# Kernel optimization log

Hardware: AMD Instinct MI355X
Metric: run time of the kernel (lower is better)

Reference implementation:

```python
import jax, jax.numpy as jnp
import numpy as np

BLOCK_LEN = 64

def _segsum(x):
    # x: (..., T) -> (..., T, T) with entry [t, s] = sum_{u=s+1..t} x[u], -inf above diagonal
    T = x.shape[-1]
    cs = jnp.cumsum(x, axis=-1)
    ss = cs[..., :, None] - cs[..., None, :]
    mask = jnp.tril(jnp.ones((T, T), dtype=bool))
    return jnp.where(mask, ss, -jnp.inf)

def setup_inputs() -> dict:
    key = jax.random.key(0)
    kx, ka, kb, kc = jax.random.split(key, 4)
    b, L, h, p, n = 4, 4096, 32, 64, 16
    X = jax.random.normal(kx, (b, L, h, p), dtype=jnp.float32)
    # negative, small-magnitude A so exp(cumsum(A)) stays finite (decaying SSM),
    # matching the math of the module while keeping the baseline numerically sane
    A = -0.1 * jnp.abs(jax.random.normal(ka, (b, L, h), dtype=jnp.float32))
    B = jax.random.normal(kb, (b, L, h, n), dtype=jnp.float32)
    C = jax.random.normal(kc, (b, L, h, n), dtype=jnp.float32)
    return {"X": X, "A": A, "B": B, "C": C}

def reference(X, A, B, C):
    b, L, h, p = X.shape
    n = B.shape[-1]
    l = BLOCK_LEN
    c = L // l
    # chunk into blocks
    Xb = X.reshape(b, c, l, h, p)                       # b c l h p
    Ab = A.reshape(b, c, l, h).transpose(0, 3, 1, 2)    # b h c l
    Bb = B.reshape(b, c, l, h, n)                       # b c l h n
    Cb = C.reshape(b, c, l, h, n)                       # b c l h n
    A_cumsum = jnp.cumsum(Ab, axis=-1)                  # b h c l
    # intra-chunk (diagonal) term; equals the fused per-timestep scan
    # h_t = exp(A_t)*h_{t-1} + B_t*x_t ; y_t = C_t . h_t
    Lmat = jnp.exp(_segsum(Ab))                         # b h c l l (lower-tri)
    Y_diag = jnp.einsum('bclhn,bcshn,bhcls,bcshp->bclhp', Cb, Bb, Lmat, Xb)
    # per-chunk end states
    decay_states = jnp.exp(A_cumsum[..., -1:] - A_cumsum)  # b h c l
    states = jnp.einsum('bclhn,bhcl,bclhp->bchpn', Bb, decay_states, Xb)
    states = jnp.concatenate([jnp.zeros_like(states[:, :1]), states], axis=1)  # b (c+1) h p n
    # inter-chunk recurrence via segment-sum of chunk totals
    decay_chunk = jnp.exp(_segsum(jnp.pad(A_cumsum[..., -1], ((0, 0), (0, 0), (1, 0)))))  # b h (c+1) (c+1)
    new_states = jnp.einsum('bhzc,bchpn->bzhpn', decay_chunk, states)
    states = new_states[:, :-1]                          # b c h p n
    # state -> output contribution
    state_decay_out = jnp.exp(A_cumsum)                  # b h c l
    Y_off = jnp.einsum('bclhn,bchpn,bhcl->bclhp', Cb, states, state_decay_out)
    return (Y_diag + Y_off).reshape(b, L, h, p)
```

## Files before the change

kernel.cpp:

```cpp
#include <hip/hip_runtime.h>

#define BATCH   4
#define SEQLEN  4096
#define NHEADS  32
#define PDIM    64
#define NDIM    16
#define CHUNK   64
#define NCHUNK  64
#define PHALF   32

typedef short v8s __attribute__((ext_vector_type(8)));
typedef float v4f __attribute__((ext_vector_type(4)));

union V8U { v8s s; unsigned u[4]; };

__device__ __forceinline__ short f2bf(float f) {
    union { float f; unsigned u; } x; x.f = f;
    unsigned r = (x.u + 0x7FFFu + ((x.u >> 16) & 1u)) >> 16;
    return (short)r;
}
__device__ __forceinline__ float bf2f(short s) {
    union { unsigned u; float f; } x; x.u = ((unsigned)(unsigned short)s) << 16;
    return x.f;
}
__device__ __forceinline__ unsigned cvt_pk_bf16(float lo, float hi) {
    unsigned r;
    asm("v_cvt_pk_bf16_f32 %0, %1, %2" : "=v"(r) : "v"(lo), "v"(hi));
    return r;
}

__device__ __forceinline__ float wave_iscan(float v, int lane) {
#pragma unroll
    for (int d = 1; d < 64; d <<= 1) {
        float o = __shfl_up(v, (unsigned)d, 64);
        if (lane >= d) v += o;
    }
    return v;
}

__global__ __launch_bounds__(512) void k_fused(
    const float* __restrict__ X, const float* __restrict__ A,
    const float* __restrict__ Bm, const float* __restrict__ Cm,
    float* __restrict__ Y)
{
    const int ph = blockIdx.x, hh = blockIdx.y, bb = blockIdx.z;
    const int tid = threadIdx.x;
    const int lane = tid & 63;
    const int wv = tid >> 6;
    const int W = wv & 3;
    const int qq = lane >> 4, nn = lane & 15;

    __shared__ __align__(16) short xF [2][4][64][8];
    __shared__ __align__(16) short xSF[2][4][64][8];
    __shared__ __align__(16) short cFq[2][2048];
    __shared__ __align__(16) short bFq[2][2048];
    __shared__ __align__(16) short bFs[2][1024];
    __shared__ __align__(16) short sF [2][1024];
    __shared__ __align__(16) float gRaw[CHUNK][68];
    __shared__ float sCum[2][CHUNK];

    {
        const v8s z8 = {0,0,0,0,0,0,0,0};
        ((v8s*)cFq)[tid] = z8;
        ((v8s*)bFq)[tid] = z8;
        if (tid < 256) ((v8s*)sF)[tid] = z8;
    }

    auto stage = [&](int c, int buf) {
        const int t0c = bb * SEQLEN + c * CHUNK;
        const float af = A[(size_t)(t0c + lane) * NHEADS + hh];
        float cum = wave_iscan(af, lane);
        const float tot = __shfl(cum, 63, 64);
        if (wv == 4) sCum[buf][lane] = cum;
        const float dec_own = __expf(tot - cum);
        const int ti = wv - 4;
        const int kk = ti >> 1, nt = ti & 1;
        const int p = ph * PHALF + nt * 16 + nn;
        const float* xb = X + ((size_t)(t0c + kk * 32 + qq * 8) * NHEADS + hh) * PDIM + p;
        float xv[8];
#pragma unroll
        for (int j = 0; j < 8; ++j) xv[j] = xb[(size_t)j * NHEADS * PDIM];
        float dv[8];
#pragma unroll
        for (int j = 0; j < 8; ++j) dv[j] = __shfl(dec_own, kk * 32 + qq * 8 + j, 64);
        V8U xf, xs;
#pragma unroll
        for (int j2 = 0; j2 < 4; ++j2) {
            xf.u[j2] = cvt_pk_bf16(xv[2*j2], xv[2*j2+1]);
            xs.u[j2] = cvt_pk_bf16(xv[2*j2] * dv[2*j2], xv[2*j2+1] * dv[2*j2+1]);
        }
        *(v8s*)&xF [buf][kk*2+nt][lane][0] = xf.s;
        *(v8s*)&xSF[buf][kk*2+nt][lane][0] = xs.s;
        const int ptid = tid & 255;
        const int r = ptid >> 2, n0 = (ptid & 3) * 4;
        const float4 bv = *(const float4*)&Bm[((size_t)(t0c + r) * NHEADS + hh) * NDIM + n0];
        const int offq = ((r >> 4) * 64 + (n0 >> 3) * 16 + (r & 15)) * 8 + (n0 & 7);
        bFq[buf][offq + 0] = f2bf(bv.x); bFq[buf][offq + 1] = f2bf(bv.y);
        bFq[buf][offq + 2] = f2bf(bv.z); bFq[buf][offq + 3] = f2bf(bv.w);
        const int kb = r >> 5, qb = (r >> 3) & 3, jj = r & 7;
        const int bs = (kb * 64 + qb * 16) * 8 + jj;
        bFs[buf][bs + (n0 + 0) * 8] = f2bf(bv.x);
        bFs[buf][bs + (n0 + 1) * 8] = f2bf(bv.y);
        bFs[buf][bs + (n0 + 2) * 8] = f2bf(bv.z);
        bFs[buf][bs + (n0 + 3) * 8] = f2bf(bv.w);
        const float4 cv = *(const float4*)&Cm[((size_t)(t0c + r) * NHEADS + hh) * NDIM + n0];
        cFq[buf][offq + 0] = f2bf(cv.x); cFq[buf][offq + 1] = f2bf(cv.y);
        cFq[buf][offq + 2] = f2bf(cv.z); cFq[buf][offq + 3] = f2bf(cv.w);
    };

    __syncthreads();
    if (wv >= 4) stage(0, 0);
    __syncthreads();

    v4f S = {0.f, 0.f, 0.f, 0.f};
    const v4f zero = {0.f, 0.f, 0.f, 0.f};

#pragma unroll 1
    for (int k = 0; k < NCHUNK; ++k) {
        const int cur = k & 1;
        if (wv >= 4) {
            if (k + 1 < NCHUNK) stage(k + 1, cur ^ 1);
        } else {
            const int t0c = bb * SEQLEN + k * CHUNK;
            const float* scm = &sCum[cur][0];
            float tcum[4];
#pragma unroll
            for (int r = 0; r < 4; ++r) tcum[r] = scm[W * 16 + qq * 4 + r];
            const v8s cfrag = *(const v8s*)&cFq[cur][(W * 64 + lane) * 8];

#pragma unroll
            for (int st = 0; st < 4; ++st) {
                if (st <= W) {
                    const v8s bfrag = *(const v8s*)&bFq[cur][(st * 64 + lane) * 8];
                    v4f acc = __builtin_amdgcn_mfma_f32_16x16x32_bf16(cfrag, bfrag, zero, 0, 0, 0);
                    const float cums = scm[st * 16 + nn];
#pragma unroll
                    for (int r = 0; r < 4; ++r) {
                        const int t = W * 16 + qq * 4 + r;
                        const int s = st * 16 + nn;
                        gRaw[t][s] = (t >= s) ? acc[r] * __expf(tcum[r] - cums) : 0.f;
                    }
                }
            }
            if (W == 0) {
#pragma unroll
                for (int r = 0; r < 4; ++r) gRaw[qq * 4 + r][16 + nn] = 0.f;
            } else if (W == 2) {
#pragma unroll
                for (int r = 0; r < 4; ++r) gRaw[32 + qq * 4 + r][48 + nn] = 0.f;
            }

            const float et = __expf(scm[W * 16 + nn]);
            V8U cef;
#pragma unroll
            for (int j2 = 0; j2 < 4; ++j2)
                cef.u[j2] = cvt_pk_bf16(bf2f(cfrag[2*j2]) * et, bf2f(cfrag[2*j2+1]) * et);

            V8U ga0u, ga1u;
            {
                const float* gr = &gRaw[W * 16 + nn][qq * 8];
#pragma unroll
                for (int j2 = 0; j2 < 4; ++j2) ga0u.u[j2] = cvt_pk_bf16(gr[2*j2], gr[2*j2+1]);
            }
            const bool usekk1 = (W >= 2);
            if (usekk1) {
                const float* gr = &gRaw[W * 16 + nn][32 + qq * 8];
#pragma unroll
                for (int j2 = 0; j2 < 4; ++j2) ga1u.u[j2] = cvt_pk_bf16(gr[2*j2], gr[2*j2+1]);
            }

            v4f ya[2];
#pragma unroll
            for (int nt2 = 0; nt2 < 2; ++nt2) {
                const v8s sfrag = *(const v8s*)&sF[cur][(nt2 * 64 + lane) * 8];
                v4f a = __builtin_amdgcn_mfma_f32_16x16x32_bf16(cef.s, sfrag, zero, 0, 0, 0);
                const v8s x0 = *(const v8s*)&xF[cur][0 + nt2][lane][0];
                a = __builtin_amdgcn_mfma_f32_16x16x32_bf16(ga0u.s, x0, a, 0, 0, 0);
                if (usekk1) {
                    const v8s x1 = *(const v8s*)&xF[cur][2 + nt2][lane][0];
                    a = __builtin_amdgcn_mfma_f32_16x16x32_bf16(ga1u.s, x1, a, 0, 0, 0);
                }
                ya[nt2] = a;
            }
#pragma unroll
            for (int r = 0; r < 4; ++r) {
                const int t = W * 16 + qq * 4 + r;
                float* yp = Y + ((size_t)(t0c + t) * NHEADS + hh) * PDIM + ph * PHALF + nn;
                yp[0]  = ya[0][r];
                yp[16] = ya[1][r];
            }

            if (W < 2) {
                const v8s a0 = *(const v8s*)&xSF[cur][0 + W][lane][0];
                const v8s a1 = *(const v8s*)&xSF[cur][2 + W][lane][0];
                const v8s b0 = *(const v8s*)&bFs[cur][(0 * 64 + lane) * 8];
                const v8s b1 = *(const v8s*)&bFs[cur][(1 * 64 + lane) * 8];
                v4f sa = __builtin_amdgcn_mfma_f32_16x16x32_bf16(a0, b0, zero, 0, 0, 0);
                sa = __builtin_amdgcn_mfma_f32_16x16x32_bf16(a1, b1, sa, 0, 0, 0);
                const float Et = __expf(scm[63]);
#pragma unroll
                for (int r = 0; r < 4; ++r) S[r] = Et * S[r] + sa[r];
                short* d = &sF[cur ^ 1][0];
#pragma unroll
                for (int r = 0; r < 4; ++r)
                    d[(W * 64 + (nn >> 3) * 16 + qq * 4 + r) * 8 + (nn & 7)] = f2bf(S[r]);
            }
        }
        __syncthreads();
    }
}

extern "C" void kernel_launch(void* const* d_in, const int* in_sizes, int n_in,
                              void* d_out, int out_size, void* d_ws, size_t ws_size,
                              hipStream_t stream) {
    const float* X  = (const float*)d_in[0];
    const float* A  = (const float*)d_in[1];
    const float* Bm = (const float*)d_in[2];
    const float* Cm = (const float*)d_in[3];
    float* Y = (float*)d_out;
    (void)d_ws; (void)ws_size;

    dim3 grid(2, NHEADS, BATCH);
    k_fused<<<grid, 512, 0, stream>>>(X, A, Bm, Cm, Y);
}
```

Baseline: 336.1 us.

## Split P into quarters, precompute full A cumsum, specialize staging waves

Doubles the grid by splitting the P dimension into four 16-wide slices, so each block handles a quarter of the head dimension and the workgroup count rises from 256 to 512. The cumulative sum of A over the whole sequence is computed once per block into shared memory, replacing the per-chunk wave scans, and chunk decays are formed relative to the previous chunk's cumsum. The staging waves are reassigned: two load X, one loads B and one loads C using contiguous float4 loads. In exchange, the per-chunk B·C gram MFMA work and the B/C loads are duplicated across twice as many blocks, and a global cumsum may lose float precision over long sequences.

```diff
diff --git a/kernel.cpp b/kernel.cpp
--- a/kernel.cpp
+++ b/kernel.cpp
@@ -7,7 +7,7 @@
 #define NDIM    16
 #define CHUNK   64
 #define NCHUNK  64
-#define PHALF   32
+#define PQ      16
 
 typedef short v8s __attribute__((ext_vector_type(8)));
 typedef float v4f __attribute__((ext_vector_type(4)));
@@ -50,65 +50,102 @@
     const int W = wv & 3;
     const int qq = lane >> 4, nn = lane & 15;
 
-    __shared__ __align__(16) short xF [2][4][64][8];
-    __shared__ __align__(16) short xSF[2][4][64][8];
+    __shared__ __align__(16) float sCumAll[SEQLEN];
+    __shared__ __align__(16) short xF [2][2][64][8];
+    __shared__ __align__(16) short xSF[2][2][64][8];
     __shared__ __align__(16) short cFq[2][2048];
     __shared__ __align__(16) short bFq[2][2048];
     __shared__ __align__(16) short bFs[2][1024];
-    __shared__ __align__(16) short sF [2][1024];
+    __shared__ __align__(16) short sF [2][512];
     __shared__ __align__(16) float gRaw[CHUNK][68];
-    __shared__ float sCum[2][CHUNK];
+    __shared__ float wtot[8];
 
     {
         const v8s z8 = {0,0,0,0,0,0,0,0};
         ((v8s*)cFq)[tid] = z8;
         ((v8s*)bFq)[tid] = z8;
-        if (tid < 256) ((v8s*)sF)[tid] = z8;
+        if (tid < 128) ((v8s*)sF)[tid] = z8;
+    }
+
+    {
+        const float* Ab = A + (size_t)bb * SEQLEN * NHEADS + hh;
+        const int tb = wv * 512 + lane * 8;
+        float av[8];
+#pragma unroll
+        for (int j = 0; j < 8; ++j) av[j] = Ab[(size_t)(tb + j) * NHEADS];
+        float s8 = 0.f;
+#pragma unroll
+        for (int j = 0; j < 8; ++j) s8 += av[j];
+        const float pre = wave_iscan(s8, lane);
+        if (lane == 63) wtot[wv] = pre;
+        __syncthreads();
+        float base = 0.f;
+#pragma unroll
+        for (int w = 0; w < 7; ++w) if (w < wv) base += wtot[w];
+        float c = base + pre - s8;
+#pragma unroll
+        for (int j = 0; j < 8; ++j) { c += av[j]; sCumAll[tb + j] = c; }
+        __syncthreads();
     }
 
     auto stage = [&](int c, int buf) {
         const int t0c = bb * SEQLEN + c * CHUNK;
-        const float af = A[(size_t)(t0c + lane) * NHEADS + hh];
-        float cum = wave_iscan(af, lane);
-        const float tot = __shfl(cum, 63, 64);
-        if (wv == 4) sCum[buf][lane] = cum;
-        const float dec_own = __expf(tot - cum);
-        const int ti = wv - 4;
-        const int kk = ti >> 1, nt = ti & 1;
-        const int p = ph * PHALF + nt * 16 + nn;
-        const float* xb = X + ((size_t)(t0c + kk * 32 + qq * 8) * NHEADS + hh) * PDIM + p;
-        float xv[8];
-#pragma unroll
-        for (int j = 0; j < 8; ++j) xv[j] = xb[(size_t)j * NHEADS * PDIM];
-        float dv[8];
-#pragma unroll
-        for (int j = 0; j < 8; ++j) dv[j] = __shfl(dec_own, kk * 32 + qq * 8 + j, 64);
-        V8U xf, xs;
-#pragma unroll
-        for (int j2 = 0; j2 < 4; ++j2) {
-            xf.u[j2] = cvt_pk_bf16(xv[2*j2], xv[2*j2+1]);
-            xs.u[j2] = cvt_pk_bf16(xv[2*j2] * dv[2*j2], xv[2*j2+1] * dv[2*j2+1]);
+        const float* gcc = &sCumAll[c * CHUNK];
+        if (wv <= 5) {
+            const int kk = wv - 4;
+            const int trow = kk * 32 + qq * 8;
+            const float* xb = X + ((size_t)(t0c + trow) * NHEADS + hh) * PDIM + ph * PQ + nn;
+            float xv[8];
+#pragma unroll
+            for (int j = 0; j < 8; ++j) xv[j] = xb[(size_t)j * (NHEADS * PDIM)];
+            const float gtot = gcc[63];
+            float ex[8];
+#pragma unroll
+            for (int j = 0; j < 8; ++j) ex[j] = __expf(gtot - gcc[trow + j]);
+            V8U xf, xs;
+#pragma unroll
+            for (int j2 = 0; j2 < 4; ++j2) {
+                xf.u[j2] = cvt_pk_bf16(xv[2*j2], xv[2*j2+1]);
+                xs.u[j2] = cvt_pk_bf16(xv[2*j2] * ex[2*j2], xv[2*j2+1] * ex[2*j2+1]);
+            }
+            *(v8s*)&xF [buf][kk][lane][0] = xf.s;
+            *(v8s*)&xSF[buf][kk][lane][0] = xs.s;
+        } else if (wv == 6) {
+            const float* bp = &Bm[((size_t)(t0c + lane) * NHEADS + hh) * NDIM];
+            const float4 v0 = *(const float4*)(bp);
+            const float4 v1 = *(const float4*)(bp + 4);
+            const float4 v2 = *(const float4*)(bp + 8);
+            const float4 v3 = *(const float4*)(bp + 12);
+            V8U lo, hi;
+            lo.u[0] = cvt_pk_bf16(v0.x, v0.y); lo.u[1] = cvt_pk_bf16(v0.z, v0.w);
+            lo.u[2] = cvt_pk_bf16(v1.x, v1.y); lo.u[3] = cvt_pk_bf16(v1.z, v1.w);
+            hi.u[0] = cvt_pk_bf16(v2.x, v2.y); hi.u[1] = cvt_pk_bf16(v2.z, v2.w);
+            hi.u[2] = cvt_pk_bf16(v3.x, v3.y); hi.u[3] = cvt_pk_bf16(v3.z, v3.w);
+            const int off0 = ((lane >> 4) * 64 + (lane & 15)) * 8;
+            *(v8s*)&bFq[buf][off0]       = lo.s;
+            *(v8s*)&bFq[buf][off0 + 128] = hi.s;
+            const int bs = ((lane >> 5) * 64 + ((lane >> 3) & 3) * 16) * 8 + (lane & 7);
+#pragma unroll
+            for (int n = 0; n < 8; ++n) bFs[buf][bs + n * 8]       = lo.s[n];
+#pragma unroll
+            for (int n = 0; n < 8; ++n) bFs[buf][bs + (n + 8) * 8] = hi.s[n];
+        } else {
+            const float* cp = &Cm[((size_t)(t0c + lane) * NHEADS + hh) * NDIM];
+            const float4 v0 = *(const float4*)(cp);
+            const float4 v1 = *(const float4*)(cp + 4);
+            const float4 v2 = *(const float4*)(cp + 8);
+            const float4 v3 = *(const float4*)(cp + 12);
+            V8U lo, hi;
+            lo.u[0] = cvt_pk_bf16(v0.x, v0.y); lo.u[1] = cvt_pk_bf16(v0.z, v0.w);
+            lo.u[2] = cvt_pk_bf16(v1.x, v1.y); lo.u[3] = cvt_pk_bf16(v1.z, v1.w);
+            hi.u[0] = cvt_pk_bf16(v2.x, v2.y); hi.u[1] = cvt_pk_bf16(v2.z, v2.w);
+            hi.u[2] = cvt_pk_bf16(v3.x, v3.y); hi.u[3] = cvt_pk_bf16(v3.z, v3.w);
+            const int off0 = ((lane >> 4) * 64 + (lane & 15)) * 8;
+            *(v8s*)&cFq[buf][off0]       = lo.s;
+            *(v8s*)&cFq[buf][off0 + 128] = hi.s;
         }
-        *(v8s*)&xF [buf][kk*2+nt][lane][0] = xf.s;
-        *(v8s*)&xSF[buf][kk*2+nt][lane][0] = xs.s;
-        const int ptid = tid & 255;
-        const int r = ptid >> 2, n0 = (ptid & 3) * 4;
-        const float4 bv = *(const float4*)&Bm[((size_t)(t0c + r) * NHEADS + hh) * NDIM + n0];
-        const int offq = ((r >> 4) * 64 + (n0 >> 3) * 16 + (r & 15)) * 8 + (n0 & 7);
-        bFq[buf][offq + 0] = f2bf(bv.x); bFq[buf][offq + 1] = f2bf(bv.y);
-        bFq[buf][offq + 2] = f2bf(bv.z); bFq[buf][offq + 3] = f2bf(bv.w);
-        const int kb = r >> 5, qb = (r >> 3) & 3, jj = r & 7;
-        const int bs = (kb * 64 + qb * 16) * 8 + jj;
-        bFs[buf][bs + (n0 + 0) * 8] = f2bf(bv.x);
-        bFs[buf][bs + (n0 + 1) * 8] = f2bf(bv.y);
-        bFs[buf][bs + (n0 + 2) * 8] = f2bf(bv.z);
-        bFs[buf][bs + (n0 + 3) * 8] = f2bf(bv.w);
-        const float4 cv = *(const float4*)&Cm[((size_t)(t0c + r) * NHEADS + hh) * NDIM + n0];
-        cFq[buf][offq + 0] = f2bf(cv.x); cFq[buf][offq + 1] = f2bf(cv.y);
-        cFq[buf][offq + 2] = f2bf(cv.z); cFq[buf][offq + 3] = f2bf(cv.w);
     };
 
-    __syncthreads();
     if (wv >= 4) stage(0, 0);
     __syncthreads();
 
@@ -122,10 +159,11 @@
             if (k + 1 < NCHUNK) stage(k + 1, cur ^ 1);
         } else {
             const int t0c = bb * SEQLEN + k * CHUNK;
-            const float* scm = &sCum[cur][0];
+            const float* gc = &sCumAll[k * CHUNK];
+            const float gbase = (k == 0) ? 0.f : gc[-1];
             float tcum[4];
 #pragma unroll
-            for (int r = 0; r < 4; ++r) tcum[r] = scm[W * 16 + qq * 4 + r];
+            for (int r = 0; r < 4; ++r) tcum[r] = gc[W * 16 + qq * 4 + r];
             const v8s cfrag = *(const v8s*)&cFq[cur][(W * 64 + lane) * 8];
 
 #pragma unroll
@@ -133,7 +171,7 @@
                 if (st <= W) {
                     const v8s bfrag = *(const v8s*)&bFq[cur][(st * 64 + lane) * 8];
                     v4f acc = __builtin_amdgcn_mfma_f32_16x16x32_bf16(cfrag, bfrag, zero, 0, 0, 0);
-                    const float cums = scm[st * 16 + nn];
+                    const float cums = gc[st * 16 + nn];
 #pragma unroll
                     for (int r = 0; r < 4; ++r) {
                         const int t = W * 16 + qq * 4 + r;
@@ -150,7 +188,7 @@
                 for (int r = 0; r < 4; ++r) gRaw[32 + qq * 4 + r][48 + nn] = 0.f;
             }
 
-            const float et = __expf(scm[W * 16 + nn]);
+            const float et = __expf(gc[W * 16 + nn] - gbase);
             V8U cef;
 #pragma unroll
             for (int j2 = 0; j2 < 4; ++j2)
@@ -169,41 +207,34 @@
                 for (int j2 = 0; j2 < 4; ++j2) ga1u.u[j2] = cvt_pk_bf16(gr[2*j2], gr[2*j2+1]);
             }
 
-            v4f ya[2];
-#pragma unroll
-            for (int nt2 = 0; nt2 < 2; ++nt2) {
-                const v8s sfrag = *(const v8s*)&sF[cur][(nt2 * 64 + lane) * 8];
-                v4f a = __builtin_amdgcn_mfma_f32_16x16x32_bf16(cef.s, sfrag, zero, 0, 0, 0);
-                const v8s x0 = *(const v8s*)&xF[cur][0 + nt2][lane][0];
-                a = __builtin_amdgcn_mfma_f32_16x16x32_bf16(ga0u.s, x0, a, 0, 0, 0);
-                if (usekk1) {
-                    const v8s x1 = *(const v8s*)&xF[cur][2 + nt2][lane][0];
-                    a = __builtin_amdgcn_mfma_f32_16x16x32_bf16(ga1u.s, x1, a, 0, 0, 0);
-                }
-                ya[nt2] = a;
+            const v8s sfrag = *(const v8s*)&sF[cur][lane * 8];
+            v4f a = __builtin_amdgcn_mfma_f32_16x16x32_bf16(cef.s, sfrag, zero, 0, 0, 0);
+            const v8s x0 = *(const v8s*)&xF[cur][0][lane][0];
+            a = __builtin_amdgcn_mfma_f32_16x16x32_bf16(ga0u.s, x0, a, 0, 0, 0);
+            if (usekk1) {
+                const v8s x1 = *(const v8s*)&xF[cur][1][lane][0];
+                a = __builtin_amdgcn_mfma_f32_16x16x32_bf16(ga1u.s, x1, a, 0, 0, 0);
             }
 #pragma unroll
             for (int r = 0; r < 4; ++r) {
                 const int t = W * 16 + qq * 4 + r;
-                float* yp = Y + ((size_t)(t0c + t) * NHEADS + hh) * PDIM + ph * PHALF + nn;
-                yp[0]  = ya[0][r];
-                yp[16] = ya[1][r];
-            }
-
-            if (W < 2) {
-                const v8s a0 = *(const v8s*)&xSF[cur][0 + W][lane][0];
-                const v8s a1 = *(const v8s*)&xSF[cur][2 + W][lane][0];
+                Y[((size_t)(t0c + t) * NHEADS + hh) * PDIM + ph * PQ + nn] = a[r];
+            }
+
+            if (W == 0) {
+                const v8s a0 = *(const v8s*)&xSF[cur][0][lane][0];
+                const v8s a1 = *(const v8s*)&xSF[cur][1][lane][0];
                 const v8s b0 = *(const v8s*)&bFs[cur][(0 * 64 + lane) * 8];
                 const v8s b1 = *(const v8s*)&bFs[cur][(1 * 64 + lane) * 8];
                 v4f sa = __builtin_amdgcn_mfma_f32_16x16x32_bf16(a0, b0, zero, 0, 0, 0);
                 sa = __builtin_amdgcn_mfma_f32_16x16x32_bf16(a1, b1, sa, 0, 0, 0);
-                const float Et = __expf(scm[63]);
+                const float Et = __expf(gc[63] - gbase);
 #pragma unroll
                 for (int r = 0; r < 4; ++r) S[r] = Et * S[r] + sa[r];
                 short* d = &sF[cur ^ 1][0];
 #pragma unroll
                 for (int r = 0; r < 4; ++r)
-                    d[(W * 64 + (nn >> 3) * 16 + qq * 4 + r) * 8 + (nn & 7)] = f2bf(S[r]);
+                    d[((nn >> 3) * 16 + qq * 4 + r) * 8 + (nn & 7)] = f2bf(S[r]);
             }
         }
         __syncthreads();
@@ -220,6 +251,6 @@
     float* Y = (float*)d_out;
     (void)d_ws; (void)ws_size;
 
-    dim3 grid(2, NHEADS, BATCH);
+    dim3 grid(4, NHEADS, BATCH);
     k_fused<<<grid, 512, 0, stream>>>(X, A, Bm, Cm, Y);
 }
```

Measured after the change: 367.4 us. 1.09x slower.

## Precompute global A cumsum, process chunk pairs with balanced triangular work and 4-deep buffers

Applied to the files above, without the earlier changes.

Computes the cumulative sum of A for the whole sequence once into shared memory, replacing the per-chunk wave scans in staging. The compute waves now handle two chunks per iteration: each wave builds the triangular G block for chunk A at row W and for chunk B at row 3-W, which balances the triangular MFMA work across waves. The state recurrence for both chunks runs before chunk B's output. Buffers go from double to quadruple, staging runs two chunks ahead, and s_setprio raises compute wave priority. Exponents now use differences from a global cumsum, so precision depends on that running sum, and shared memory use grows substantially.

```diff
diff --git a/kernel.cpp b/kernel.cpp
--- a/kernel.cpp
+++ b/kernel.cpp
@@ -50,44 +50,64 @@
     const int W = wv & 3;
     const int qq = lane >> 4, nn = lane & 15;
 
-    __shared__ __align__(16) short xF [2][4][64][8];
-    __shared__ __align__(16) short xSF[2][4][64][8];
-    __shared__ __align__(16) short cFq[2][2048];
-    __shared__ __align__(16) short bFq[2][2048];
-    __shared__ __align__(16) short bFs[2][1024];
-    __shared__ __align__(16) short sF [2][1024];
-    __shared__ __align__(16) float gRaw[CHUNK][68];
-    __shared__ float sCum[2][CHUNK];
+    __shared__ __align__(16) float sCumAll[SEQLEN];
+    __shared__ __align__(16) short xF [4][4][64][8];
+    __shared__ __align__(16) short xSF[4][4][64][8];
+    __shared__ __align__(16) short cFq[4][2048];
+    __shared__ __align__(16) short bFq[4][2048];
+    __shared__ __align__(16) short bFs[4][1024];
+    __shared__ __align__(16) short sF [4][1024];
+    __shared__ __align__(16) float gRawA[CHUNK][68];
+    __shared__ __align__(16) float gRawB[CHUNK][68];
+    __shared__ float wtot[8];
 
     {
         const v8s z8 = {0,0,0,0,0,0,0,0};
-        ((v8s*)cFq)[tid] = z8;
-        ((v8s*)bFq)[tid] = z8;
-        if (tid < 256) ((v8s*)sF)[tid] = z8;
+        ((v8s*)cFq)[tid] = z8; ((v8s*)cFq)[tid + 512] = z8;
+        ((v8s*)bFq)[tid] = z8; ((v8s*)bFq)[tid + 512] = z8;
+        if (tid < 128) ((v8s*)sF)[tid] = z8;
+    }
+
+    {
+        const float* Ab = A + (size_t)bb * SEQLEN * NHEADS + hh;
+        const int tb = wv * 512 + lane * 8;
+        float av[8];
+#pragma unroll
+        for (int j = 0; j < 8; ++j) av[j] = Ab[(size_t)(tb + j) * NHEADS];
+        float s8 = 0.f;
+#pragma unroll
+        for (int j = 0; j < 8; ++j) s8 += av[j];
+        const float pre = wave_iscan(s8, lane);
+        if (lane == 63) wtot[wv] = pre;
+        __syncthreads();
+        float base = 0.f;
+#pragma unroll
+        for (int w = 0; w < 7; ++w) if (w < wv) base += wtot[w];
+        float c = base + pre - s8;
+#pragma unroll
+        for (int j = 0; j < 8; ++j) { c += av[j]; sCumAll[tb + j] = c; }
+        __syncthreads();
     }
 
     auto stage = [&](int c, int buf) {
         const int t0c = bb * SEQLEN + c * CHUNK;
-        const float af = A[(size_t)(t0c + lane) * NHEADS + hh];
-        float cum = wave_iscan(af, lane);
-        const float tot = __shfl(cum, 63, 64);
-        if (wv == 4) sCum[buf][lane] = cum;
-        const float dec_own = __expf(tot - cum);
-        const int ti = wv - 4;
-        const int kk = ti >> 1, nt = ti & 1;
-        const int p = ph * PHALF + nt * 16 + nn;
-        const float* xb = X + ((size_t)(t0c + kk * 32 + qq * 8) * NHEADS + hh) * PDIM + p;
+        const float* gcc = &sCumAll[c * CHUNK];
+        const int ti = wv - 4, kk = ti >> 1, nt = ti & 1;
+        const int trow = kk * 32 + qq * 8;
+        const float* xb = X + ((size_t)(t0c + trow) * NHEADS + hh) * PDIM
+                            + ph * PHALF + nt * 16 + nn;
         float xv[8];
 #pragma unroll
-        for (int j = 0; j < 8; ++j) xv[j] = xb[(size_t)j * NHEADS * PDIM];
-        float dv[8];
-#pragma unroll
-        for (int j = 0; j < 8; ++j) dv[j] = __shfl(dec_own, kk * 32 + qq * 8 + j, 64);
+        for (int j = 0; j < 8; ++j) xv[j] = xb[(size_t)j * (NHEADS * PDIM)];
+        const float gtot = gcc[63];
+        float ex[8];
+#pragma unroll
+        for (int j = 0; j < 8; ++j) ex[j] = __expf(gtot - gcc[trow + j]);
         V8U xf, xs;
 #pragma unroll
         for (int j2 = 0; j2 < 4; ++j2) {
             xf.u[j2] = cvt_pk_bf16(xv[2*j2], xv[2*j2+1]);
-            xs.u[j2] = cvt_pk_bf16(xv[2*j2] * dv[2*j2], xv[2*j2+1] * dv[2*j2+1]);
+            xs.u[j2] = cvt_pk_bf16(xv[2*j2] * ex[2*j2], xv[2*j2+1] * ex[2*j2+1]);
         }
         *(v8s*)&xF [buf][kk*2+nt][lane][0] = xf.s;
         *(v8s*)&xSF[buf][kk*2+nt][lane][0] = xs.s;
@@ -108,103 +128,130 @@
         cFq[buf][offq + 2] = f2bf(cv.z); cFq[buf][offq + 3] = f2bf(cv.w);
     };
 
-    __syncthreads();
-    if (wv >= 4) stage(0, 0);
-    __syncthreads();
-
-    v4f S = {0.f, 0.f, 0.f, 0.f};
     const v4f zero = {0.f, 0.f, 0.f, 0.f};
 
-#pragma unroll 1
-    for (int k = 0; k < NCHUNK; ++k) {
-        const int cur = k & 1;
-        if (wv >= 4) {
-            if (k + 1 < NCHUNK) stage(k + 1, cur ^ 1);
-        } else {
-            const int t0c = bb * SEQLEN + k * CHUNK;
-            const float* scm = &sCum[cur][0];
-            float tcum[4];
-#pragma unroll
-            for (int r = 0; r < 4; ++r) tcum[r] = scm[W * 16 + qq * 4 + r];
-            const v8s cfrag = *(const v8s*)&cFq[cur][(W * 64 + lane) * 8];
-
-#pragma unroll
-            for (int st = 0; st < 4; ++st) {
-                if (st <= W) {
-                    const v8s bfrag = *(const v8s*)&bFq[cur][(st * 64 + lane) * 8];
-                    v4f acc = __builtin_amdgcn_mfma_f32_16x16x32_bf16(cfrag, bfrag, zero, 0, 0, 0);
-                    const float cums = scm[st * 16 + nn];
-#pragma unroll
-                    for (int r = 0; r < 4; ++r) {
-                        const int t = W * 16 + qq * 4 + r;
-                        const int s = st * 16 + nn;
-                        gRaw[t][s] = (t >= s) ? acc[r] * __expf(tcum[r] - cums) : 0.f;
-                    }
+    auto qk_g = [&](float (*gR)[68], const float* gc, int buf, int tau) -> v8s {
+        const v8s cfrag = *(const v8s*)&cFq[buf][(tau * 64 + lane) * 8];
+        float tc[4];
+#pragma unroll
+        for (int r = 0; r < 4; ++r) tc[r] = gc[tau * 16 + qq * 4 + r];
+#pragma unroll
+        for (int st = 0; st < 4; ++st) {
+            if (st <= tau) {
+                const v8s bfrag = *(const v8s*)&bFq[buf][(st * 64 + lane) * 8];
+                v4f acc = __builtin_amdgcn_mfma_f32_16x16x32_bf16(cfrag, bfrag, zero, 0, 0, 0);
+                const float cums = gc[st * 16 + nn];
+#pragma unroll
+                for (int r = 0; r < 4; ++r) {
+                    const int t = tau * 16 + qq * 4 + r;
+                    const int s = st * 16 + nn;
+                    gR[t][s] = (t >= s) ? acc[r] * __expf(tc[r] - cums) : 0.f;
                 }
             }
-            if (W == 0) {
-#pragma unroll
-                for (int r = 0; r < 4; ++r) gRaw[qq * 4 + r][16 + nn] = 0.f;
-            } else if (W == 2) {
-#pragma unroll
-                for (int r = 0; r < 4; ++r) gRaw[32 + qq * 4 + r][48 + nn] = 0.f;
+        }
+        if (tau == 0) {
+#pragma unroll
+            for (int r = 0; r < 4; ++r) gR[qq * 4 + r][16 + nn] = 0.f;
+        } else if (tau == 2) {
+#pragma unroll
+            for (int r = 0; r < 4; ++r) gR[32 + qq * 4 + r][48 + nn] = 0.f;
+        }
+        return cfrag;
+    };
+
+    auto do_y = [&](float (*gR)[68], const float* gc, float gbase, int buf,
+                    int t0c, v8s cfrag) {
+        const float et = __expf(gc[W * 16 + nn] - gbase);
+        V8U cef;
+#pragma unroll
+        for (int j2 = 0; j2 < 4; ++j2)
+            cef.u[j2] = cvt_pk_bf16(bf2f(cfrag[2*j2]) * et, bf2f(cfrag[2*j2+1]) * et);
+        V8U ga0u, ga1u;
+        {
+            const float* gr = &gR[W * 16 + nn][qq * 8];
+#pragma unroll
+            for (int j2 = 0; j2 < 4; ++j2) ga0u.u[j2] = cvt_pk_bf16(gr[2*j2], gr[2*j2+1]);
+        }
+        const bool usekk1 = (W >= 2);
+        if (usekk1) {
+            const float* gr = &gR[W * 16 + nn][32 + qq * 8];
+#pragma unroll
+            for (int j2 = 0; j2 < 4; ++j2) ga1u.u[j2] = cvt_pk_bf16(gr[2*j2], gr[2*j2+1]);
+        }
+        v4f ya[2];
+#pragma unroll
+        for (int nt2 = 0; nt2 < 2; ++nt2) {
+            const v8s sfrag = *(const v8s*)&sF[buf][(nt2 * 64 + lane) * 8];
+            v4f a = __builtin_amdgcn_mfma_f32_16x16x32_bf16(cef.s, sfrag, zero, 0, 0, 0);
+            const v8s x0 = *(const v8s*)&xF[buf][0 + nt2][lane][0];
+            a = __builtin_amdgcn_mfma_f32_16x16x32_bf16(ga0u.s, x0, a, 0, 0, 0);
+            if (usekk1) {
+                const v8s x1 = *(const v8s*)&xF[buf][2 + nt2][lane][0];
+                a = __builtin_amdgcn_mfma_f32_16x16x32_bf16(ga1u.s, x1, a, 0, 0, 0);
             }
-
-            const float et = __expf(scm[W * 16 + nn]);
-            V8U cef;
-#pragma unroll
-            for (int j2 = 0; j2 < 4; ++j2)
-                cef.u[j2] = cvt_pk_bf16(bf2f(cfrag[2*j2]) * et, bf2f(cfrag[2*j2+1]) * et);
-
-            V8U ga0u, ga1u;
-            {
-                const float* gr = &gRaw[W * 16 + nn][qq * 8];
-#pragma unroll
-                for (int j2 = 0; j2 < 4; ++j2) ga0u.u[j2] = cvt_pk_bf16(gr[2*j2], gr[2*j2+1]);
+            ya[nt2] = a;
+        }
+#pragma unroll
+        for (int r = 0; r < 4; ++r) {
+            const int t = W * 16 + qq * 4 + r;
+            float* yp = Y + ((size_t)(t0c + t) * NHEADS + hh) * PDIM + ph * PHALF + nn;
+            yp[0]  = ya[0][r];
+            yp[16] = ya[1][r];
+        }
+    };
+
+    auto do_state = [&](int buf, float Et, int pub, v4f& S) {
+        const v8s a0 = *(const v8s*)&xSF[buf][0 + W][lane][0];
+        const v8s a1 = *(const v8s*)&xSF[buf][2 + W][lane][0];
+        const v8s b0 = *(const v8s*)&bFs[buf][(0 * 64 + lane) * 8];
+        const v8s b1 = *(const v8s*)&bFs[buf][(1 * 64 + lane) * 8];
+        v4f sa = __builtin_amdgcn_mfma_f32_16x16x32_bf16(a0, b0, zero, 0, 0, 0);
+        sa = __builtin_amdgcn_mfma_f32_16x16x32_bf16(a1, b1, sa, 0, 0, 0);
+#pragma unroll
+        for (int r = 0; r < 4; ++r) S[r] = Et * S[r] + sa[r];
+        short* d = &sF[pub][0];
+#pragma unroll
+        for (int r = 0; r < 4; ++r)
+            d[(W * 64 + (nn >> 3) * 16 + qq * 4 + r) * 8 + (nn & 7)] = f2bf(S[r]);
+    };
+
+    if (wv >= 4) { stage(0, 0); stage(1, 1); }
+    __syncthreads();
+
+    v4f S = {0.f, 0.f, 0.f, 0.f};
+    v8s cfragB = {0,0,0,0,0,0,0,0};
+
+#pragma unroll 1
+    for (int k = 0; k < NCHUNK; k += 2) {
+        const int bufA = k & 3, bufB = (k + 1) & 3;
+        const float* gcA = &sCumAll[k * CHUNK];
+        const float* gcB = gcA + CHUNK;
+
+        if (wv >= 4) {
+            if (k + 2 < NCHUNK) stage(k + 2, (k + 2) & 3);
+        } else {
+            __builtin_amdgcn_s_setprio(1);
+            const float gbaseA = (k == 0) ? 0.f : gcA[-1];
+            const int t0cA = bb * SEQLEN + k * CHUNK;
+            const v8s cfragA = qk_g(gRawA, gcA, bufA, W);
+            qk_g(gRawB, gcB, bufB, 3 - W);
+            do_y(gRawA, gcA, gbaseA, bufA, t0cA, cfragA);
+            if (W < 2) {
+                do_state(bufA, __expf(gcA[63] - gbaseA), bufB, S);
+                do_state(bufB, __expf(gcB[63] - gcA[63]), (k + 2) & 3, S);
             }
-            const bool usekk1 = (W >= 2);
-            if (usekk1) {
-                const float* gr = &gRaw[W * 16 + nn][32 + qq * 8];
-#pragma unroll
-                for (int j2 = 0; j2 < 4; ++j2) ga1u.u[j2] = cvt_pk_bf16(gr[2*j2], gr[2*j2+1]);
-            }
-
-            v4f ya[2];
-#pragma unroll
-            for (int nt2 = 0; nt2 < 2; ++nt2) {
-                const v8s sfrag = *(const v8s*)&sF[cur][(nt2 * 64 + lane) * 8];
-                v4f a = __builtin_amdgcn_mfma_f32_16x16x32_bf16(cef.s, sfrag, zero, 0, 0, 0);
-                const v8s x0 = *(const v8s*)&xF[cur][0 + nt2][lane][0];
-                a = __builtin_amdgcn_mfma_f32_16x16x32_bf16(ga0u.s, x0, a, 0, 0, 0);
-                if (usekk1) {
-                    const v8s x1 = *(const v8s*)&xF[cur][2 + nt2][lane][0];
-                    a = __builtin_amdgcn_mfma_f32_16x16x32_bf16(ga1u.s, x1, a, 0, 0, 0);
-                }
-                ya[nt2] = a;
-            }
-#pragma unroll
-            for (int r = 0; r < 4; ++r) {
-                const int t = W * 16 + qq * 4 + r;
-                float* yp = Y + ((size_t)(t0c + t) * NHEADS + hh) * PDIM + ph * PHALF + nn;
-                yp[0]  = ya[0][r];
-                yp[16] = ya[1][r];
-            }
-
-            if (W < 2) {
-                const v8s a0 = *(const v8s*)&xSF[cur][0 + W][lane][0];
-                const v8s a1 = *(const v8s*)&xSF[cur][2 + W][lane][0];
-                const v8s b0 = *(const v8s*)&bFs[cur][(0 * 64 + lane) * 8];
-                const v8s b1 = *(const v8s*)&bFs[cur][(1 * 64 + lane) * 8];
-                v4f sa = __builtin_amdgcn_mfma_f32_16x16x32_bf16(a0, b0, zero, 0, 0, 0);
-                sa = __builtin_amdgcn_mfma_f32_16x16x32_bf16(a1, b1, sa, 0, 0, 0);
-                const float Et = __expf(scm[63]);
-#pragma unroll
-                for (int r = 0; r < 4; ++r) S[r] = Et * S[r] + sa[r];
-                short* d = &sF[cur ^ 1][0];
-#pragma unroll
-                for (int r = 0; r < 4; ++r)
-                    d[(W * 64 + (nn >> 3) * 16 + qq * 4 + r) * 8 + (nn & 7)] = f2bf(S[r]);
-            }
+            __builtin_amdgcn_s_setprio(0);
+        }
+        __syncthreads();
+
+        if (wv >= 4) {
+            if (k + 3 < NCHUNK) stage(k + 3, (k + 3) & 3);
+        } else {
+            __builtin_amdgcn_s_setprio(1);
+            const int t0cB = bb * SEQLEN + (k + 1) * CHUNK;
+            cfragB = *(const v8s*)&cFq[bufB][(W * 64 + lane) * 8];
+            do_y(gRawB, gcB, gcA[63], bufB, t0cB, cfragB);
+            __builtin_amdgcn_s_setprio(0);
         }
         __syncthreads();
     }
```

Result: faster. 308.3 us (-8.3%).
